# Kernel optimization log

Hardware: AMD Instinct MI355X
Metric: run time of the kernel (lower is better)

The kernel has to match this reference:

```python
import jax, jax.numpy as jnp
import numpy as np

R = 2          # sparse sampler stride (AvgPool2d kernel=1, stride=r == strided subsample)
HEADS = 8
CHANNELS = 512
HEAD_DIM = CHANNELS // HEADS


def setup_inputs() -> dict:
    key = jax.random.key(0)
    k1, k2 = jax.random.split(key)
    x = jax.random.normal(k1, (2, CHANNELS, 112, 112), dtype=jnp.float32)
    # 1x1 conv weight, bias=False: [out=3C, in=C]
    w_qkv = jax.random.normal(k2, (3 * CHANNELS, CHANNELS), dtype=jnp.float32) * (CHANNELS ** -0.5)
    return {"x": x, "w_qkv": w_qkv}


def reference(x, w_qkv):
    # sparse_sampler: AvgPool2d(kernel_size=1, stride=R) == strided subsampling
    x = x[:, :, ::R, ::R]
    B, C, H, W = x.shape
    N = H * W
    # 1x1 conv -> [B, 3C, H, W]
    qkv = jnp.einsum('oc,bchw->bohw', w_qkv, x)
    # view(B, heads, 3*head_dim, N): per-head contiguous [q|k|v] chunks
    qkv = qkv.reshape(B, HEADS, 3 * HEAD_DIM, N)
    q, k, v = jnp.split(qkv, 3, axis=2)  # each [B, heads, head_dim, N]
    # attn = (q^T @ k).softmax(-1)  -- NOTE: scale is defined but NOT applied in the original
    attn = jax.nn.softmax(jnp.einsum('bhdn,bhdm->bhnm', q, k), axis=-1)  # [B,h,N,N]
    # out = v @ attn^T : out[d, m] = sum_n v[d, n] * attn[m, n]
    out = jnp.einsum('bhdn,bhmn->bhdm', v, attn)  # [B,h,head_dim,N]
    return out.reshape(B, C, H, W)
```

## Files before the change

### kernel.cpp

```cpp
#include <hip/hip_runtime.h>

#define N_TOK 3136
#define WOUT 56
#define CH 512
#define HD 64
#define LOG2E 1.44269504088896340736f

typedef _Float16 h4 __attribute__((ext_vector_type(4)));
typedef _Float16 h8 __attribute__((ext_vector_type(8)));
typedef float f32x4 __attribute__((ext_vector_type(4)));
typedef float f32x16 __attribute__((ext_vector_type(16)));
typedef unsigned u32x2 __attribute__((ext_vector_type(2)));
typedef unsigned u32x4 __attribute__((ext_vector_type(4)));

#define WS_XH 0
#define WS_WF 3211264
#define WS_QT 3997696
#define WS_KT 7208960
#define WS_VW 10420224
#define WS_PO13 13631488
#define WS_ML 23265280
#define SPLIT_O 3211264
#define ML_N 200704

__device__ inline unsigned pkh(float a, float b) {
    return __builtin_bit_cast(unsigned, __builtin_amdgcn_cvt_pkrtz(a, b));
}
__device__ inline float fexp2(float x) {
#if __has_builtin(__builtin_amdgcn_exp2f)
    return __builtin_amdgcn_exp2f(x);
#else
    float r;
    asm("v_exp_f32 %0, %1" : "=v"(r) : "v"(x));
    return r;
#endif
}
__device__ inline void plswap(unsigned& a, unsigned& b) {
#if __has_builtin(__builtin_amdgcn_permlane32_swap)
    u32x2 r = __builtin_amdgcn_permlane32_swap(a, b, false, false);
    a = r.x; b = r.y;
#else
    unsigned a2 = (unsigned)__shfl_xor((int)a, 32);
    unsigned b2 = (unsigned)__shfl_xor((int)b, 32);
    bool hi = (threadIdx.x & 63) >= 32;
    unsigned na = hi ? b2 : a;
    unsigned nb = hi ? b : a2;
    a = na; b = nb;
#endif
}

__global__ __launch_bounds__(256) void k_ds(const float* __restrict__ x,
                                            const float* __restrict__ w,
                                            _Float16* __restrict__ xh,
                                            _Float16* __restrict__ wf) {
    const int t = threadIdx.x;
    if (blockIdx.y == 8) {
        int base = (blockIdx.z * 49 + blockIdx.x) * 8192 + t;
        #pragma unroll 8
        for (int i = 0; i < 32; ++i) {
            int idx = base + i * 256;
            if (idx < 1536 * 512) wf[idx] = (_Float16)w[idx];
        }
        return;
    }
    __shared__ float tile[64 * 65];
    const int q = t >> 6, l = t & 63;
    const int n0 = blockIdx.x * 64, c0 = blockIdx.y * 64, b = blockIdx.z;
    #pragma unroll
    for (int r = 0; r < 16; ++r) {
        int c_l = q * 16 + r;
        int n = n0 + l;
        int hh = n / WOUT, ww = n - hh * WOUT;
        tile[c_l * 65 + l] =
            x[(((size_t)(b * CH + c0 + c_l)) * 112 + hh * 2) * 112 + ww * 2];
    }
    __syncthreads();
    #pragma unroll
    for (int r = 0; r < 16; ++r) {
        int n_l = q * 16 + r;
        xh[((size_t)b * N_TOK + n0 + n_l) * CH + c0 + l] = (_Float16)tile[l * 65 + n_l];
    }
}

__global__ __launch_bounds__(256) void k_proj(const _Float16* __restrict__ wf,
                                              const _Float16* __restrict__ xh,
                                              _Float16* __restrict__ qT,
                                              _Float16* __restrict__ kT,
                                              _Float16* __restrict__ vW) {
    __shared__ __align__(16) _Float16 Wt[64 * 72];
    __shared__ __align__(16) _Float16 Xh[64 * 72];
    const int t = threadIdx.x;
    const int n0 = blockIdx.x * 64, o0 = blockIdx.y * 64, b = blockIdx.z;
    const int w = t >> 6, L = t & 63, lm = L & 15, g = L >> 4;
    const int wo = w >> 1, wn = w & 1;
    const int sr = t >> 2, sc = (t & 3) * 8;

    f32x4 acc[2][2] = {};
    for (int kc = 0; kc < 8; ++kc) {
        const int c0 = kc * 64;
        const size_t wbase = (size_t)(o0 + sr) * CH + c0 + sc;
        const size_t xbase = ((size_t)b * N_TOK + n0 + sr) * CH + c0 + sc;
        h8 rw0 = *(const h8*)&wf[wbase], rw1 = *(const h8*)&wf[wbase + 32];
        h8 rh0 = *(const h8*)&xh[xbase], rh1 = *(const h8*)&xh[xbase + 32];
        __syncthreads();
        *(h8*)&Wt[sr * 72 + sc] = rw0; *(h8*)&Wt[sr * 72 + sc + 32] = rw1;
        *(h8*)&Xh[sr * 72 + sc] = rh0; *(h8*)&Xh[sr * 72 + sc + 32] = rh1;
        __syncthreads();
        #pragma unroll
        for (int kk2 = 0; kk2 < 2; ++kk2) {
            const int kb = kk2 * 32 + g * 8;
            h8 a0 = *(h8*)&Wt[(wo * 32 + lm) * 72 + kb];
            h8 a1 = *(h8*)&Wt[(wo * 32 + 16 + lm) * 72 + kb];
            h8 b0 = *(h8*)&Xh[(wn * 32 + lm) * 72 + kb];
            h8 b1 = *(h8*)&Xh[(wn * 32 + 16 + lm) * 72 + kb];
            acc[0][0] = __builtin_amdgcn_mfma_f32_16x16x32_f16(a0, b0, acc[0][0], 0, 0, 0);
            acc[0][1] = __builtin_amdgcn_mfma_f32_16x16x32_f16(a0, b1, acc[0][1], 0, 0, 0);
            acc[1][0] = __builtin_amdgcn_mfma_f32_16x16x32_f16(a1, b0, acc[1][0], 0, 0, 0);
            acc[1][1] = __builtin_amdgcn_mfma_f32_16x16x32_f16(a1, b1, acc[1][1], 0, 0, 0);
        }
    }
    #pragma unroll
    for (int ot = 0; ot < 2; ++ot) {
        int obase = o0 + wo * 32 + ot * 16;
        int h = obase / 192;
        int typ = (obase / 64) % 3;
        int dbase = (wo * 32 + ot * 16) & 63;
        #pragma unroll
        for (int nt = 0; nt < 2; ++nt) {
            int n = n0 + wn * 32 + nt * 16 + lm;
            f32x4 a = acc[ot][nt];
            if (typ == 2) {
                #pragma unroll
                for (int j = 0; j < 4; ++j)
                    vW[((size_t)(b * 8 + h) * HD + dbase + g * 4 + j) * N_TOK + n] = (_Float16)a[j];
            } else if (typ == 1) {
                h4 hv = {(_Float16)(a[0] * LOG2E), (_Float16)(a[1] * LOG2E),
                         (_Float16)(a[2] * LOG2E), (_Float16)(a[3] * LOG2E)};
                *(h4*)&kT[((size_t)(b * 8 + h) * N_TOK + n) * HD + dbase + g * 4] = hv;
            } else {
                h4 hv = {(_Float16)a[0], (_Float16)a[1], (_Float16)a[2], (_Float16)a[3]};
                *(h4*)&qT[((size_t)(b * 8 + h) * N_TOK + n) * HD + dbase + g * 4] = hv;
            }
        }
    }
}

__global__ __launch_bounds__(256, 2) void k_attn(const _Float16* __restrict__ qT,
                                                 const _Float16* __restrict__ kT,
                                                 const _Float16* __restrict__ vW,
                                                 _Float16* __restrict__ wsbase,
                                                 float* __restrict__ pm,
                                                 float* __restrict__ pl) {
    __shared__ __align__(16) _Float16 Ks[64 * 72];
    __shared__ __align__(16) _Float16 Vs[64 * 72];

    const int t = threadIdx.x;
    const int w = t >> 6, L = t & 63, lm = L & 31, hi = L >> 5;

    const int lin = blockIdx.x + 25 * blockIdx.y + 400 * blockIdx.z;
    const int nl = (lin & 7) * 200 + (lin >> 3);
    const int combo = nl / 25;
    const int mt = nl - combo * 25;
    const int bh = combo & 15;
    const int split = combo >> 4;
    const int qbase = (mt == 24) ? (N_TOK - 128) : mt * 128;
    const int mw = qbase + w * 32;

    const int cs = split * 12 + (split > 0 ? 1 : 0);
    const int ce = cs + (split == 0 ? 13 : 12);

    const size_t qb = ((size_t)bh * N_TOK + mw + lm) * HD;
    h8 qf[4];
    #pragma unroll
    for (int ks = 0; ks < 4; ++ks) qf[ks] = *(const h8*)&qT[qb + ks * 16 + hi * 8];

    const int sr = t >> 2;
    const int scol = (t & 3) * 16;
    const _Float16* ka = kT + (size_t)bh * N_TOK * HD + (size_t)(cs * 64 + sr) * HD + scol;
    const _Float16* va = vW + (size_t)bh * HD * N_TOK + (size_t)sr * N_TOK + cs * 64 + scol;

    float m_run = -1e30f, l_run = 0.f;
    f32x16 o_acc[2] = {};

    {
        h8 pk0 = *(const h8*)&ka[0], pk1 = *(const h8*)&ka[8];
        h8 pv0 = *(const h8*)&va[0], pv1 = *(const h8*)&va[8];
        ka += 64 * HD; va += 64;
        *(h8*)&Ks[sr * 72 + scol] = pk0; *(h8*)&Ks[sr * 72 + scol + 8] = pk1;
        *(h8*)&Vs[sr * 72 + scol] = pv0; *(h8*)&Vs[sr * 72 + scol + 8] = pv1;
    }
    __syncthreads();

    for (int ch = cs; ch < ce; ++ch) {
        const bool pf = (ch + 1 < ce);
        h8 pk0, pk1, pv0, pv1;
        if (pf) {
            pk0 = *(const h8*)&ka[0]; pk1 = *(const h8*)&ka[8];
            pv0 = *(const h8*)&va[0]; pv1 = *(const h8*)&va[8];
            ka += 64 * HD; va += 64;
        }

        f32x16 s0 = {}, s1 = {};
        __builtin_amdgcn_s_setprio(1);
        #pragma unroll
        for (int ks = 0; ks < 4; ++ks) {
            h8 a0 = *(const h8*)&Ks[lm * 72 + ks * 16 + hi * 8];
            h8 a1 = *(const h8*)&Ks[(32 + lm) * 72 + ks * 16 + hi * 8];
            s0 = __builtin_amdgcn_mfma_f32_32x32x16_f16(a0, qf[ks], s0, 0, 0, 0);
            s1 = __builtin_amdgcn_mfma_f32_32x32x16_f16(a1, qf[ks], s1, 0, 0, 0);
        }
        __builtin_amdgcn_s_setprio(0);

        float cmax = -1e30f;
        #pragma unroll
        for (int r = 0; r < 16; ++r) cmax = fmaxf(cmax, fmaxf(s0[r], s1[r]));
        cmax = fmaxf(cmax, __shfl_xor(cmax, 32));
        if (!__all(cmax - m_run <= 7.f)) {
            float mnew = fmaxf(m_run, cmax);
            float alpha = fexp2(m_run - mnew);
            m_run = mnew;
            l_run *= alpha;
            #pragma unroll
            for (int r = 0; r < 16; ++r) { o_acc[0][r] *= alpha; o_acc[1][r] *= alpha; }
        }
        float p[2][16];
        float psum = 0.f;
        #pragma unroll
        for (int r = 0; r < 16; ++r) {
            p[0][r] = fexp2(s0[r] - m_run);
            p[1][r] = fexp2(s1[r] - m_run);
            psum += p[0][r] + p[1][r];
        }
        psum += __shfl_xor(psum, 32);
        l_run += psum;

        h8 pfrag[4];
        #pragma unroll
        for (int kt = 0; kt < 2; ++kt) {
            #pragma unroll
            for (int half = 0; half < 2; ++half) {
                const int b0 = half * 8;
                unsigned w01 = pkh(p[kt][b0 + 0], p[kt][b0 + 1]);
                unsigned w23 = pkh(p[kt][b0 + 2], p[kt][b0 + 3]);
                unsigned w45 = pkh(p[kt][b0 + 4], p[kt][b0 + 5]);
                unsigned w67 = pkh(p[kt][b0 + 6], p[kt][b0 + 7]);
                plswap(w01, w45);
                plswap(w23, w67);
                u32x4 uu = {w01, w23, w45, w67};
                pfrag[kt * 2 + half] = __builtin_bit_cast(h8, uu);
            }
        }

        __builtin_amdgcn_s_setprio(1);
        #pragma unroll
        for (int ns = 0; ns < 4; ++ns) {
            h8 av0 = *(const h8*)&Vs[lm * 72 + ns * 16 + hi * 8];
            h8 av1 = *(const h8*)&Vs[(32 + lm) * 72 + ns * 16 + hi * 8];
            o_acc[0] = __builtin_amdgcn_mfma_f32_32x32x16_f16(av0, pfrag[ns], o_acc[0], 0, 0, 0);
            o_acc[1] = __builtin_amdgcn_mfma_f32_32x32x16_f16(av1, pfrag[ns], o_acc[1], 0, 0, 0);
        }
        __builtin_amdgcn_s_setprio(0);

        if (pf) {
            __syncthreads();
            *(h8*)&Ks[sr * 72 + scol] = pk0; *(h8*)&Ks[sr * 72 + scol + 8] = pk1;
            *(h8*)&Vs[sr * 72 + scol] = pv0; *(h8*)&Vs[sr * 72 + scol + 8] = pv1;
            __syncthreads();
        }
    }

    float inv = 1.0f / l_run;
    _Float16* pO = (split == 0) ? wsbase
                                : wsbase + WS_PO13 + (size_t)(split - 1) * SPLIT_O;
    const size_t pob = (size_t)bh * HD * N_TOK + mw + lm;
    #pragma unroll
    for (int dt = 0; dt < 2; ++dt)
        #pragma unroll
        for (int r = 0; r < 16; ++r) {
            int d = dt * 32 + (r & 3) + 8 * (r >> 2) + 4 * hi;
            pO[pob + (size_t)d * N_TOK] = (_Float16)(o_acc[dt][r] * inv);
        }
    if (hi == 0) {
        pm[(split * 16 + bh) * N_TOK + mw + lm] = m_run;
        pl[(split * 16 + bh) * N_TOK + mw + lm] = l_run;
    }
}

__global__ __launch_bounds__(256) void k_comb(const _Float16* __restrict__ wsbase,
                                              const float* __restrict__ pm,
                                              const float* __restrict__ pl,
                                              float* __restrict__ out) {
    int idx = blockIdx.x * 256 + threadIdx.x;
    int n = idx % N_TOK;
    int bh = (idx / N_TOK) >> 6;
    float m[4], l[4];
    #pragma unroll
    for (int s = 0; s < 4; ++s) {
        m[s] = pm[(s * 16 + bh) * N_TOK + n];
        l[s] = pl[(s * 16 + bh) * N_TOK + n];
    }
    float mm = fmaxf(fmaxf(m[0], m[1]), fmaxf(m[2], m[3]));
    float num = 0.f, den = 0.f;
    #pragma unroll
    for (int s = 0; s < 4; ++s) {
        const _Float16* pO = (s == 0) ? wsbase
                                      : wsbase + WS_PO13 + (size_t)(s - 1) * SPLIT_O;
        float wg = fexp2(m[s] - mm) * l[s];
        num += (float)pO[idx] * wg;
        den += wg;
    }
    out[idx] = num / den;
}

extern "C" void kernel_launch(void* const* d_in, const int* in_sizes, int n_in,
                              void* d_out, int out_size, void* d_ws, size_t ws_size,
                              hipStream_t stream) {
    const float* x = (const float*)d_in[0];
    const float* wq = (const float*)d_in[1];
    float* out = (float*)d_out;
    _Float16* ws = (_Float16*)d_ws;

    _Float16* xh = ws + WS_XH;
    _Float16* wf = ws + WS_WF;
    _Float16* qT = ws + WS_QT;
    _Float16* kT = ws + WS_KT;
    _Float16* vW = ws + WS_VW;
    float* pm = (float*)(ws + WS_ML);
    float* pl = pm + ML_N;

    k_ds<<<dim3(49, 9, 2), 256, 0, stream>>>(x, wq, xh, wf);
    k_proj<<<dim3(49, 24, 2), 256, 0, stream>>>(wf, xh, qT, kT, vW);
    k_attn<<<dim3(25, 16, 4), 256, 0, stream>>>(qT, kT, vW, ws, pm, pl);
    k_comb<<<dim3(12544), 256, 0, stream>>>(ws, pm, pl, out);
}
```

Before: 129.2 us.

## Enlarge projection GEMM tiles to 128x128 and defer softmax max rescale

The projection kernel moves from 64x64 to 128x128 output tiles. Each wave now computes a 32x128 slab, which raises operand reuse per LDS load and cuts the block count; the last token tile overlaps the previous one so 3136 tokens are covered. In attention, exponentials are computed with the old running max first, and the max/rescale path runs only when a partial row sum exceeds a threshold. That skips the per-tile max reduction at the cost of occasionally recomputing exponentials, and it depends on fp16 P values staying in range.

```diff
diff --git a/kernel.cpp b/kernel.cpp
--- a/kernel.cpp
+++ b/kernel.cpp
@@ -87,47 +87,56 @@
                                               _Float16* __restrict__ qT,
                                               _Float16* __restrict__ kT,
                                               _Float16* __restrict__ vW) {
-    __shared__ __align__(16) _Float16 Wt[64 * 72];
-    __shared__ __align__(16) _Float16 Xh[64 * 72];
+    __shared__ __align__(16) _Float16 Wt[128 * 72];
+    __shared__ __align__(16) _Float16 Xt[128 * 72];
     const int t = threadIdx.x;
-    const int n0 = blockIdx.x * 64, o0 = blockIdx.y * 64, b = blockIdx.z;
+    const int mtn = blockIdx.x;
+    const int n0 = (mtn == 24) ? (N_TOK - 128) : mtn * 128;
+    const int o0 = blockIdx.y * 128;
+    const int b = blockIdx.z;
     const int w = t >> 6, L = t & 63, lm = L & 15, g = L >> 4;
-    const int wo = w >> 1, wn = w & 1;
-    const int sr = t >> 2, sc = (t & 3) * 8;
-
-    f32x4 acc[2][2] = {};
+    const int sr = t >> 1, sc = (t & 1) * 32;
+
+    f32x4 acc[2][8] = {};
     for (int kc = 0; kc < 8; ++kc) {
         const int c0 = kc * 64;
-        const size_t wbase = (size_t)(o0 + sr) * CH + c0 + sc;
-        const size_t xbase = ((size_t)b * N_TOK + n0 + sr) * CH + c0 + sc;
-        h8 rw0 = *(const h8*)&wf[wbase], rw1 = *(const h8*)&wf[wbase + 32];
-        h8 rh0 = *(const h8*)&xh[xbase], rh1 = *(const h8*)&xh[xbase + 32];
+        const size_t wb = (size_t)(o0 + sr) * CH + c0 + sc;
+        const size_t xb = ((size_t)b * N_TOK + n0 + sr) * CH + c0 + sc;
+        h8 rw[4], rx[4];
+        #pragma unroll
+        for (int i = 0; i < 4; ++i) {
+            rw[i] = *(const h8*)&wf[wb + i * 8];
+            rx[i] = *(const h8*)&xh[xb + i * 8];
+        }
         __syncthreads();
-        *(h8*)&Wt[sr * 72 + sc] = rw0; *(h8*)&Wt[sr * 72 + sc + 32] = rw1;
-        *(h8*)&Xh[sr * 72 + sc] = rh0; *(h8*)&Xh[sr * 72 + sc + 32] = rh1;
+        #pragma unroll
+        for (int i = 0; i < 4; ++i) {
+            *(h8*)&Wt[sr * 72 + sc + i * 8] = rw[i];
+            *(h8*)&Xt[sr * 72 + sc + i * 8] = rx[i];
+        }
         __syncthreads();
         #pragma unroll
         for (int kk2 = 0; kk2 < 2; ++kk2) {
             const int kb = kk2 * 32 + g * 8;
-            h8 a0 = *(h8*)&Wt[(wo * 32 + lm) * 72 + kb];
-            h8 a1 = *(h8*)&Wt[(wo * 32 + 16 + lm) * 72 + kb];
-            h8 b0 = *(h8*)&Xh[(wn * 32 + lm) * 72 + kb];
-            h8 b1 = *(h8*)&Xh[(wn * 32 + 16 + lm) * 72 + kb];
-            acc[0][0] = __builtin_amdgcn_mfma_f32_16x16x32_f16(a0, b0, acc[0][0], 0, 0, 0);
-            acc[0][1] = __builtin_amdgcn_mfma_f32_16x16x32_f16(a0, b1, acc[0][1], 0, 0, 0);
-            acc[1][0] = __builtin_amdgcn_mfma_f32_16x16x32_f16(a1, b0, acc[1][0], 0, 0, 0);
-            acc[1][1] = __builtin_amdgcn_mfma_f32_16x16x32_f16(a1, b1, acc[1][1], 0, 0, 0);
+            h8 a0 = *(h8*)&Wt[(w * 32 + lm) * 72 + kb];
+            h8 a1 = *(h8*)&Wt[(w * 32 + 16 + lm) * 72 + kb];
+            #pragma unroll
+            for (int nt = 0; nt < 8; ++nt) {
+                h8 bf = *(h8*)&Xt[(nt * 16 + lm) * 72 + kb];
+                acc[0][nt] = __builtin_amdgcn_mfma_f32_16x16x32_f16(a0, bf, acc[0][nt], 0, 0, 0);
+                acc[1][nt] = __builtin_amdgcn_mfma_f32_16x16x32_f16(a1, bf, acc[1][nt], 0, 0, 0);
+            }
         }
     }
     #pragma unroll
     for (int ot = 0; ot < 2; ++ot) {
-        int obase = o0 + wo * 32 + ot * 16;
+        int obase = o0 + w * 32 + ot * 16;
         int h = obase / 192;
         int typ = (obase / 64) % 3;
-        int dbase = (wo * 32 + ot * 16) & 63;
-        #pragma unroll
-        for (int nt = 0; nt < 2; ++nt) {
-            int n = n0 + wn * 32 + nt * 16 + lm;
+        int dbase = obase & 63;
+        #pragma unroll
+        for (int nt = 0; nt < 8; ++nt) {
+            int n = n0 + nt * 16 + lm;
             f32x4 a = acc[ot][nt];
             if (typ == 2) {
                 #pragma unroll
@@ -211,25 +220,32 @@
         }
         __builtin_amdgcn_s_setprio(0);
 
-        float cmax = -1e30f;
-        #pragma unroll
-        for (int r = 0; r < 16; ++r) cmax = fmaxf(cmax, fmaxf(s0[r], s1[r]));
-        cmax = fmaxf(cmax, __shfl_xor(cmax, 32));
-        if (!__all(cmax - m_run <= 7.f)) {
+        float p[2][16];
+        float psum = 0.f;
+        #pragma unroll
+        for (int r = 0; r < 16; ++r) {
+            p[0][r] = fexp2(s0[r] - m_run);
+            p[1][r] = fexp2(s1[r] - m_run);
+            psum += p[0][r] + p[1][r];
+        }
+        if (__any(psum > 4096.f)) {
+            float cmax = -1e30f;
+            #pragma unroll
+            for (int r = 0; r < 16; ++r) cmax = fmaxf(cmax, fmaxf(s0[r], s1[r]));
+            cmax = fmaxf(cmax, __shfl_xor(cmax, 32));
             float mnew = fmaxf(m_run, cmax);
             float alpha = fexp2(m_run - mnew);
             m_run = mnew;
             l_run *= alpha;
             #pragma unroll
             for (int r = 0; r < 16; ++r) { o_acc[0][r] *= alpha; o_acc[1][r] *= alpha; }
-        }
-        float p[2][16];
-        float psum = 0.f;
-        #pragma unroll
-        for (int r = 0; r < 16; ++r) {
-            p[0][r] = fexp2(s0[r] - m_run);
-            p[1][r] = fexp2(s1[r] - m_run);
-            psum += p[0][r] + p[1][r];
+            psum = 0.f;
+            #pragma unroll
+            for (int r = 0; r < 16; ++r) {
+                p[0][r] = fexp2(s0[r] - m_run);
+                p[1][r] = fexp2(s1[r] - m_run);
+                psum += p[0][r] + p[1][r];
+            }
         }
         psum += __shfl_xor(psum, 32);
         l_run += psum;
@@ -329,7 +345,7 @@
     float* pl = pm + ML_N;
 
     k_ds<<<dim3(49, 9, 2), 256, 0, stream>>>(x, wq, xh, wf);
-    k_proj<<<dim3(49, 24, 2), 256, 0, stream>>>(wf, xh, qT, kT, vW);
+    k_proj<<<dim3(25, 12, 2), 256, 0, stream>>>(wf, xh, qT, kT, vW);
     k_attn<<<dim3(25, 16, 4), 256, 0, stream>>>(qT, kT, vW, ws, pm, pl);
     k_comb<<<dim3(12544), 256, 0, stream>>>(ws, pm, pl, out);
 }
```

After: 144.4 us. 1.12x slower.
